# Performance work log

Hardware: AMD Instinct MI355X
Metric: run time of the kernel (lower is better)

The kernel has to match this reference:

```python
import jax, jax.numpy as jnp
import numpy as np

B, T, I, H = 32, 1024, 512, 512


def _uniform(key, shape, stdv):
    return jax.random.uniform(key, shape, jnp.float32, -stdv, stdv)


def setup_inputs() -> dict:
    key = jax.random.key(0)
    ks = jax.random.split(key, 13)
    stdv = 1.0 / np.sqrt(H)
    return {
        "z": jax.random.normal(ks[0], (B, T, I, 2), jnp.float32),
        "W_zi": _uniform(ks[1], (I, H, 2), stdv), "W_hi": _uniform(ks[2], (H, H, 2), stdv), "b_i": _uniform(ks[3], (H,), stdv),
        "W_zf": _uniform(ks[4], (I, H, 2), stdv), "W_hf": _uniform(ks[5], (H, H, 2), stdv), "b_f": _uniform(ks[6], (H,), stdv),
        "W_zc": _uniform(ks[7], (I, H, 2), stdv), "W_hc": _uniform(ks[8], (H, H, 2), stdv), "b_c": _uniform(ks[9], (H, 2), stdv),
        "W_zo": _uniform(ks[10], (I, H, 2), stdv), "W_ho": _uniform(ks[11], (H, H, 2), stdv), "b_o": _uniform(ks[12], (H,), stdv),
    }


def complex_tanh(zr, zi):
    mag = jnp.maximum(jnp.sqrt(zr * zr + zi * zi + 1e-14), 1e-8)
    t = jnp.tanh(mag)
    return t * (zr / mag), t * (zi / mag)


def reference(z, W_zi, W_hi, b_i, W_zf, W_hf, b_f, W_zc, W_hc, b_c, W_zo, W_ho, b_o):
    zr, zi = z[..., 0], z[..., 1]  # (B,T,I)

    def in_proj_real(Wz):  # real part of complex matmul z @ Wz
        return jnp.einsum('bti,ih->bth', zr, Wz[..., 0]) - jnp.einsum('bti,ih->bth', zi, Wz[..., 1])

    xi = in_proj_real(W_zi)
    xf = in_proj_real(W_zf)
    xo = in_proj_real(W_zo)
    xcr = in_proj_real(W_zc)
    xci = jnp.einsum('bti,ih->bth', zi, W_zc[..., 0]) + jnp.einsum('bti,ih->bth', zr, W_zc[..., 1])

    # time-major for scan: (T,B,H)
    xs = tuple(jnp.swapaxes(a, 0, 1) for a in (xi, xf, xo, xcr, xci))

    def step(carry, x):
        h_r, h_i, c_r, c_i = carry
        xi_t, xf_t, xo_t, xcr_t, xci_t = x
        i_t = jax.nn.sigmoid(xi_t + h_r @ W_hi[..., 0] - h_i @ W_hi[..., 1] + b_i)
        f_t = jax.nn.sigmoid(xf_t + h_r @ W_hf[..., 0] - h_i @ W_hf[..., 1] + b_f)
        o_t = jax.nn.sigmoid(xo_t + h_r @ W_ho[..., 0] - h_i @ W_ho[..., 1] + b_o)
        cr = xcr_t + h_r @ W_hc[..., 0] - h_i @ W_hc[..., 1] + b_c[..., 0]
        ci = xci_t + h_i @ W_hc[..., 0] + h_r @ W_hc[..., 1] + b_c[..., 1]
        ctr, cti = complex_tanh(cr, ci)
        c_r = f_t * c_r + i_t * ctr
        c_i = f_t * c_i + i_t * cti
        hr, hi = complex_tanh(c_r, c_i)
        h_r = o_t * hr
        h_i = o_t * hi
        return (h_r, h_i, c_r, c_i), jnp.stack((h_r, h_i), axis=-1)

    zero = jnp.zeros((z.shape[0], W_hi.shape[0]), z.dtype)
    (h_r, h_i, c_r, c_i), hs = jax.lax.scan(step, (zero, zero, zero, zero), xs)
    hidden_seq = jnp.swapaxes(hs, 0, 1)  # (B,T,H,2)
    h_t = jnp.stack((h_r, h_i), axis=-1)
    c_t = jnp.stack((c_r, c_i), axis=-1)
    return hidden_seq, (h_t, c_t)
```

## Files before the change

### kernel.cpp

```cpp
#include <hip/hip_runtime.h>


#define B_ 32
#define T_ 1024
#define Hd 512
#define Kd 1024
#define Nd 2560
#define Md 32768
#define HS_ELEMS 33554432ull

typedef __attribute__((ext_vector_type(8))) short bf16x8;
typedef __attribute__((ext_vector_type(4))) float f32x4;

__device__ __forceinline__ unsigned short f_bf(float f) {
  unsigned int x; __builtin_memcpy(&x, &f, 4);
  unsigned int r = (x + 0x7FFFu + ((x >> 16) & 1u)) >> 16;
  return (unsigned short)r;
}
__device__ __forceinline__ float bf_f(unsigned short u) {
  unsigned int i = ((unsigned int)u) << 16; float f; __builtin_memcpy(&f, &i, 4); return f;
}
__device__ __forceinline__ float fsig(float x) { return 1.0f / (1.0f + __expf(-x)); }
__device__ __forceinline__ void ctanh_(float zr, float zi, float& tr, float& ti) {
  float m2 = zr * zr + zi * zi + 1e-14f;
  float mag = __fsqrt_rn(m2);
  float e = __expf(2.0f * mag);
  float th = 1.0f - 2.0f / (e + 1.0f);
  float s = th / mag;
  tr = zr * s; ti = zi * s;
}

__device__ __forceinline__ void gl16(const unsigned short* g, unsigned short* l) {
  __builtin_amdgcn_global_load_lds(
      (const __attribute__((address_space(1))) void*)g,
      (__attribute__((address_space(3))) void*)l, 16, 0, 0);
}

__device__ __forceinline__ unsigned int ald(const unsigned int* p) {
  return __hip_atomic_load(p, __ATOMIC_RELAXED, __HIP_MEMORY_SCOPE_AGENT);
}
__device__ __forceinline__ void ast(unsigned int* p, unsigned int v) {
  __hip_atomic_store(p, v, __ATOMIC_RELAXED, __HIP_MEMORY_SCOPE_AGENT);
}

__global__ void build_weights(const float* Wzi, const float* Whi, const float* bi,
                              const float* Wzf, const float* Whf, const float* bfv,
                              const float* Wzc, const float* Whc, const float* bc,
                              const float* Wzo, const float* Who, const float* bo,
                              unsigned short* WzT, unsigned short* WhT, float* bcomb) {
  int n = blockIdx.x;
  int slab = n / 80, wi = n % 80, g = wi / 16, hh = slab * 16 + (wi & 15);
  const float *Wz, *Wh;
  if (g == 0)      { Wz = Wzi; Wh = Whi; }
  else if (g == 1) { Wz = Wzf; Wh = Whf; }
  else if (g == 2) { Wz = Wzo; Wh = Who; }
  else             { Wz = Wzc; Wh = Whc; }
  int q0, q1; float s0, s1;
  if (g < 4) { q0 = 0; s0 = 1.f; q1 = 1; s1 = -1.f; }
  else       { q0 = 1; s0 = 1.f; q1 = 0; s1 =  1.f; }
  for (int k = threadIdx.x; k < Kd; k += 256) {
    int j = k >> 1, p = k & 1;
    int q = p ? q1 : q0; float sg = p ? s1 : s0;
    WzT[(size_t)n * Kd + k] = f_bf(sg * Wz[(j * Hd + hh) * 2 + q]);
    WhT[(size_t)n * Kd + k] = f_bf(sg * Wh[(j * Hd + hh) * 2 + q]);
  }
  if (threadIdx.x == 0) {
    float bv;
    if (g == 0) bv = bi[hh]; else if (g == 1) bv = bfv[hh];
    else if (g == 2) bv = bo[hh];
    else if (g == 3) bv = bc[2 * hh]; else bv = bc[2 * hh + 1];
    bcomb[n] = bv;
  }
}

__global__ void cvt_z(const float4* __restrict__ z, ushort4* __restrict__ Z2) {
  for (size_t i = (size_t)blockIdx.x * 256 + threadIdx.x; i < 8388608ull; i += 8192ull * 256) {
    float4 v = z[i];
    ushort4 o;
    o.x = f_bf(v.x); o.y = f_bf(v.y); o.z = f_bf(v.z); o.w = f_bf(v.w);
    Z2[i] = o;
  }
}

__global__ __launch_bounds__(256) void gemm_x(const unsigned short* __restrict__ Z2,
                                              const unsigned short* __restrict__ WT,
                                              unsigned short* __restrict__ X) {
  __shared__ unsigned short As[128 * 64];
  __shared__ unsigned short Bs[128 * 64];
  int tid = threadIdx.x, lane = tid & 63, wv = tid >> 6;
  int bid = blockIdx.x;
  int mb = bid / (Nd / 128), nb = bid % (Nd / 128);
  size_t m0 = (size_t)mb * 128, n0 = (size_t)nb * 128;
  int wr = wv >> 1, wc = wv & 1;
  int l15 = lane & 15, kg = lane >> 4;
  int lrow = tid >> 3;
  int lcol = (tid & 7) * 8;
  f32x4 acc[4][4] = {};
  for (int k0 = 0; k0 < Kd; k0 += 64) {
    __syncthreads();
#pragma unroll
    for (int c = 0; c < 4; ++c) {
      gl16(Z2 + (m0 + c * 32 + lrow) * Kd + k0 + lcol,
           As + (size_t)c * 2048 + wv * 512);
      gl16(WT + (n0 + c * 32 + lrow) * Kd + k0 + lcol,
           Bs + (size_t)c * 2048 + wv * 512);
    }
    __syncthreads();
#pragma unroll
    for (int ks = 0; ks < 2; ++ks) {
      int kk = ks * 32 + kg * 8;
      bf16x8 a[4], b[4];
#pragma unroll
      for (int i = 0; i < 4; ++i)
        a[i] = *reinterpret_cast<const bf16x8*>(&As[(wr * 64 + i * 16 + l15) * 64 + kk]);
#pragma unroll
      for (int j = 0; j < 4; ++j)
        b[j] = *reinterpret_cast<const bf16x8*>(&Bs[(wc * 64 + j * 16 + l15) * 64 + kk]);
#pragma unroll
      for (int i = 0; i < 4; ++i)
#pragma unroll
        for (int j = 0; j < 4; ++j)
          acc[i][j] = __builtin_amdgcn_mfma_f32_16x16x32_bf16(a[i], b[j], acc[i][j], 0, 0, 0);
    }
  }
#pragma unroll
  for (int i = 0; i < 4; ++i)
#pragma unroll
    for (int j = 0; j < 4; ++j) {
      size_t gm = m0 + wr * 64 + i * 16 + kg * 4;
      size_t gn = n0 + wc * 64 + j * 16 + l15;
#pragma unroll
      for (int r = 0; r < 4; ++r)
        X[(gm + r) * Nd + gn] = f_bf(acc[i][j][r]);
    }
}

#define CHUNK 8
#define STEPB (Nd * 2)
__global__ __launch_bounds__(512) void lstm_all(
    const unsigned short* __restrict__ WhT, const unsigned short* __restrict__ X,
    const float* __restrict__ bcomb, unsigned short* __restrict__ hb,
    int* __restrict__ flags, float* __restrict__ out) {
  __shared__ unsigned short Xs[2][CHUNK * STEPB / 2];
  __shared__ float xch[8][5][256];
  const int s = blockIdx.x;
  const int tid = threadIdx.x;
  const int wv = tid >> 6, lane = tid & 63;
  const int kh = wv >> 1, mh = wv & 1;
  const int l15 = lane & 15, kg = lane >> 4;
  const int cb = tid >> 4;
  const int ch = tid & 15;
  const int hh = s * 16 + ch;

  auto stage = [&](int tbase, int buf) {
#pragma unroll
    for (int j = 0; j < 5; ++j) {
      unsigned int P = (unsigned int)(wv * 5 + j) * 1024u + (unsigned int)lane * 16u;
      unsigned int st = P / STEPB, r = P % STEPB;
      unsigned int b = r / 160u, rem = r % 160u;
      gl16(X + ((size_t)b * T_ + (tbase + st)) * Nd + s * 80 + rem / 2,
           &Xs[buf][(size_t)(wv * 5 + j) * 512]);
    }
  };
  stage(0, 0);

  bf16x8 w[5][8];
#pragma unroll
  for (int g = 0; g < 5; ++g)
#pragma unroll
    for (int ks = 0; ks < 8; ++ks)
      w[g][ks] = *reinterpret_cast<const bf16x8*>(
          &WhT[(size_t)(s * 80 + g * 16 + l15) * Kd + kh * 256 + ks * 32 + kg * 8]);

  float bias[5];
#pragma unroll
  for (int g = 0; g < 5; ++g) bias[g] = bcomb[s * 80 + g * 16 + ch];
  float cr = 0.f, ci = 0.f;

  const int fidx = kh * 8 + (lane & 7);
  const int mb = cb >> 4;
  const int xidx = ((cb & 15) >> 2) * 64 + ch * 4 + (cb & 3);

  float2 hist[8];

  for (int tb = 0; tb < T_; tb += 8) {
#pragma unroll
    for (int j = 0; j < 8; ++j) {
      const int t = tb + j;
      bf16x8 a[8];
      if (t > 0) {
        const unsigned int need = (unsigned int)(t + 1);
        while (true) {
          unsigned int v = ald((const unsigned int*)&flags[fidx]);
          if (__all(v >= need)) break;
        }
        asm volatile("" ::: "memory");

        const unsigned short* hin = hb + (size_t)(t % 3) * 32768;
        unsigned long long hpa = (unsigned long long)(
            hin + (size_t)(mh * 16 + l15) * Kd + kh * 256 + kg * 8);
#define HL(i, off) asm volatile("global_load_dwordx4 %0, %1, off offset:" #off " sc0 sc1" \
                                 : "=&v"(a[i]) : "v"(hpa) : "memory")
        HL(0, 0); HL(1, 64); HL(2, 128); HL(3, 192);
        HL(4, 256); HL(5, 320); HL(6, 384); HL(7, 448);
#undef HL
        asm volatile("s_waitcnt vmcnt(0)" ::: "memory");
        __builtin_amdgcn_sched_barrier(0);
      } else {
#pragma unroll
        for (int ks = 0; ks < 8; ++ks)
#pragma unroll
          for (int e = 0; e < 8; ++e) a[ks][e] = 0;
      }

      f32x4 acc[5] = {};
#pragma unroll
      for (int ks = 0; ks < 8; ++ks)
#pragma unroll
        for (int g = 0; g < 5; ++g)
          acc[g] = __builtin_amdgcn_mfma_f32_16x16x32_bf16(a[ks], w[g][ks], acc[g], 0, 0, 0);

#pragma unroll
      for (int g = 0; g < 5; ++g)
        *reinterpret_cast<f32x4*>(&xch[wv][g][lane * 4]) = acc[g];
      __syncthreads();

      const unsigned short* xsl = &Xs[(t >> 3) & 1][(t & 7) * Nd + cb * 80 + ch];
      float pre[5];
#pragma unroll
      for (int g = 0; g < 5; ++g) {
        float p = bias[g] + bf_f(xsl[g * 16]);
#pragma unroll
        for (int q = 0; q < 4; ++q) p += xch[q * 2 + mb][g][xidx];
        pre[g] = p;
      }
      float ig = fsig(pre[0]), fg = fsig(pre[1]), og = fsig(pre[2]);
      float ctr, cti; ctanh_(pre[3], pre[4], ctr, cti);
      cr = fg * cr + ig * ctr;
      ci = fg * ci + ig * cti;
      float hr0, hi0; ctanh_(cr, ci, hr0, hi0);
      float hr = og * hr0, hi = og * hi0;
      hist[j] = make_float2(hr, hi);

      unsigned int hv = (unsigned int)f_bf(hr) | ((unsigned int)f_bf(hi) << 16);
      ast((unsigned int*)hb + (size_t)((t + 1) % 3) * 16384 + (size_t)cb * 512 + hh, hv);
      if (t < T_ - 1) {
        asm volatile("s_waitcnt vmcnt(0)" ::: "memory");
        __syncthreads();
        if (tid == 0) ast((unsigned int*)&flags[s], (unsigned int)(t + 2));
      }

      if (j == 7) {
#pragma unroll
        for (int q = 0; q < 8; ++q) {
          size_t oidx = ((size_t)cb * T_ + (t - 7 + q)) * (Hd * 2) + hh * 2;
          *reinterpret_cast<float2*>(&out[oidx]) = hist[q];
        }
        if (t + 1 < T_) stage(t + 1, ((t + 1) >> 3) & 1);
      }
      if (t == T_ - 1) {
        size_t fb = HS_ELEMS + ((size_t)cb * Hd + hh) * 2;
        *reinterpret_cast<float2*>(&out[fb]) = make_float2(hr, hi);
        *reinterpret_cast<float2*>(&out[fb + 32768ull]) = make_float2(cr, ci);
      }
      __syncthreads();
    }
  }
}

extern "C" void kernel_launch(void* const* d_in, const int* in_sizes, int n_in,
                              void* d_out, int out_size, void* d_ws, size_t ws_size,
                              hipStream_t stream) {
  const float* z   = (const float*)d_in[0];
  const float* Wzi = (const float*)d_in[1];
  const float* Whi = (const float*)d_in[2];
  const float* bi  = (const float*)d_in[3];
  const float* Wzf = (const float*)d_in[4];
  const float* Whf = (const float*)d_in[5];
  const float* bfv = (const float*)d_in[6];
  const float* Wzc = (const float*)d_in[7];
  const float* Whc = (const float*)d_in[8];
  const float* bc  = (const float*)d_in[9];
  const float* Wzo = (const float*)d_in[10];
  const float* Who = (const float*)d_in[11];
  const float* bo  = (const float*)d_in[12];
  float* out = (float*)d_out;

  size_t off = 0;
  char* ws = (char*)d_ws;
  auto take = [&](size_t nbytes) {
    void* p = ws + off; off += (nbytes + 255) & ~(size_t)255; return p;
  };
  unsigned short* WzT  = (unsigned short*)take((size_t)Nd * Kd * 2);
  unsigned short* WhT  = (unsigned short*)take((size_t)Nd * Kd * 2);
  float*          bcmb = (float*)take(Nd * 4);
  unsigned short* Z2   = (unsigned short*)take((size_t)Md * Kd * 2);
  unsigned short* X    = (unsigned short*)take((size_t)Md * Nd * 2);
  unsigned short* hb   = (unsigned short*)take(3 * 32768 * 2);
  int*            flags = (int*)take(64 * 4);

  hipMemsetAsync(flags, 0, 64 * 4, stream);
  build_weights<<<Nd, 256, 0, stream>>>(Wzi, Whi, bi, Wzf, Whf, bfv,
                                        Wzc, Whc, bc, Wzo, Who, bo,
                                        WzT, WhT, bcmb);
  cvt_z<<<8192, 256, 0, stream>>>((const float4*)z, (ushort4*)Z2);
  gemm_x<<<(Md / 128) * (Nd / 128), 256, 0, stream>>>(Z2, WzT, X);
  lstm_all<<<32, 512, 0, stream>>>(WhT, X, bcmb, hb, flags, out);
}
```

Before: 5.339 ms.

## Overlap input-projection GEMM with recurrent LSTM via producer blocks in one launch

Merges the input-projection GEMM into the persistent LSTM kernel. 32 blocks run the recurrence while 224 extra blocks compute X tiles in time-chunk order and signal completion per 128-step chunk through atomic counters. The GEMM cost can then hide behind the serial recurrence instead of running before it. X staging is moved to the start of each 8-step group with a wait on chunk readiness, and one per-step __syncthreads is dropped. The risks are that the GEMM blocks contend with the latency-bound recurrent blocks for bandwidth, and that the GEMM blocks now use 512 threads with only half of them active.

Result: slower. 5.703 ms (+6.8%).

```diff
diff --git a/kernel.cpp b/kernel.cpp
--- a/kernel.cpp
+++ b/kernel.cpp
@@ -82,69 +82,88 @@
   }
 }
 
-__global__ __launch_bounds__(256) void gemm_x(const unsigned short* __restrict__ Z2,
-                                              const unsigned short* __restrict__ WT,
-                                              unsigned short* __restrict__ X) {
-  __shared__ unsigned short As[128 * 64];
-  __shared__ unsigned short Bs[128 * 64];
-  int tid = threadIdx.x, lane = tid & 63, wv = tid >> 6;
-  int bid = blockIdx.x;
-  int mb = bid / (Nd / 128), nb = bid % (Nd / 128);
-  size_t m0 = (size_t)mb * 128, n0 = (size_t)nb * 128;
-  int wr = wv >> 1, wc = wv & 1;
-  int l15 = lane & 15, kg = lane >> 4;
-  int lrow = tid >> 3;
-  int lcol = (tid & 7) * 8;
-  f32x4 acc[4][4] = {};
-  for (int k0 = 0; k0 < Kd; k0 += 64) {
-    __syncthreads();
-#pragma unroll
-    for (int c = 0; c < 4; ++c) {
-      gl16(Z2 + (m0 + c * 32 + lrow) * Kd + k0 + lcol,
-           As + (size_t)c * 2048 + wv * 512);
-      gl16(WT + (n0 + c * 32 + lrow) * Kd + k0 + lcol,
-           Bs + (size_t)c * 2048 + wv * 512);
-    }
-    __syncthreads();
-#pragma unroll
-    for (int ks = 0; ks < 2; ++ks) {
-      int kk = ks * 32 + kg * 8;
-      bf16x8 a[4], b[4];
-#pragma unroll
-      for (int i = 0; i < 4; ++i)
-        a[i] = *reinterpret_cast<const bf16x8*>(&As[(wr * 64 + i * 16 + l15) * 64 + kk]);
-#pragma unroll
-      for (int j = 0; j < 4; ++j)
-        b[j] = *reinterpret_cast<const bf16x8*>(&Bs[(wc * 64 + j * 16 + l15) * 64 + kk]);
-#pragma unroll
-      for (int i = 0; i < 4; ++i)
-#pragma unroll
-        for (int j = 0; j < 4; ++j)
-          acc[i][j] = __builtin_amdgcn_mfma_f32_16x16x32_bf16(a[i], b[j], acc[i][j], 0, 0, 0);
-    }
-  }
-#pragma unroll
-  for (int i = 0; i < 4; ++i)
-#pragma unroll
-    for (int j = 0; j < 4; ++j) {
-      size_t gm = m0 + wr * 64 + i * 16 + kg * 4;
-      size_t gn = n0 + wc * 64 + j * 16 + l15;
-#pragma unroll
-      for (int r = 0; r < 4; ++r)
-        X[(gm + r) * Nd + gn] = f_bf(acc[i][j][r]);
-    }
-}
-
 #define CHUNK 8
 #define STEPB (Nd * 2)
 __global__ __launch_bounds__(512) void lstm_all(
-    const unsigned short* __restrict__ WhT, const unsigned short* __restrict__ X,
+    const unsigned short* __restrict__ WhT, unsigned short* __restrict__ X,
+    const unsigned short* __restrict__ Z2, const unsigned short* __restrict__ WzT,
     const float* __restrict__ bcomb, unsigned short* __restrict__ hb,
-    int* __restrict__ flags, float* __restrict__ out) {
+    int* __restrict__ ctl, float* __restrict__ out) {
   __shared__ unsigned short Xs[2][CHUNK * STEPB / 2];
   __shared__ float xch[8][5][256];
+  __shared__ unsigned short As[128 * 64];
+  __shared__ unsigned short Bs[128 * 64];
   const int s = blockIdx.x;
   const int tid = threadIdx.x;
+  unsigned int* bc = (unsigned int*)(ctl + 32);
+
+  if (s >= 32) {
+    const int lane = tid & 63, wvg = tid >> 6;
+    const int wr = wvg >> 1, wc = wvg & 1;
+    const int l15 = lane & 15, kg = lane >> 4;
+    const int lrow = tid >> 3;
+    const int lcol = (tid & 7) * 8;
+    for (int tau = s - 32; tau < 5120; tau += 224) {
+      int tb8 = tau / 640, rr = tau % 640;
+      int mb = (rr / 20) * 8 + tb8, nb = rr % 20;
+      size_t m0 = (size_t)mb * 128, n0 = (size_t)nb * 128;
+      f32x4 acc[4][4] = {};
+      for (int k0 = 0; k0 < Kd; k0 += 64) {
+        __syncthreads();
+        if (tid < 256) {
+#pragma unroll
+          for (int c = 0; c < 4; ++c) {
+            gl16(Z2 + (m0 + c * 32 + lrow) * Kd + k0 + lcol,
+                 As + (size_t)c * 2048 + wvg * 512);
+            gl16(WzT + (n0 + c * 32 + lrow) * Kd + k0 + lcol,
+                 Bs + (size_t)c * 2048 + wvg * 512);
+          }
+        }
+        __syncthreads();
+        if (tid < 256) {
+#pragma unroll
+          for (int ks = 0; ks < 2; ++ks) {
+            int kk = ks * 32 + kg * 8;
+            bf16x8 a[4], b[4];
+#pragma unroll
+            for (int i = 0; i < 4; ++i)
+              a[i] = *reinterpret_cast<const bf16x8*>(&As[(wr * 64 + i * 16 + l15) * 64 + kk]);
+#pragma unroll
+            for (int j = 0; j < 4; ++j)
+              b[j] = *reinterpret_cast<const bf16x8*>(&Bs[(wc * 64 + j * 16 + l15) * 64 + kk]);
+#pragma unroll
+            for (int i = 0; i < 4; ++i)
+#pragma unroll
+              for (int j = 0; j < 4; ++j)
+                acc[i][j] = __builtin_amdgcn_mfma_f32_16x16x32_bf16(a[i], b[j], acc[i][j], 0, 0, 0);
+          }
+        }
+      }
+      if (tid < 256) {
+#pragma unroll
+        for (int i = 0; i < 4; ++i)
+#pragma unroll
+          for (int j = 0; j < 4; ++j) {
+            size_t gm = m0 + wr * 64 + i * 16 + kg * 4;
+            size_t gn = n0 + wc * 64 + j * 16 + l15;
+#pragma unroll
+            for (int r = 0; r < 4; ++r) {
+              unsigned int v = f_bf(acc[i][j][r]);
+              const unsigned short* p = X + (gm + r) * Nd + gn;
+              asm volatile("global_store_short %0, %1, off sc0 sc1"
+                           :: "v"(p), "v"(v) : "memory");
+            }
+          }
+        asm volatile("s_waitcnt vmcnt(0)" ::: "memory");
+      }
+      __syncthreads();
+      if (tid == 0)
+        __hip_atomic_fetch_add((int*)&bc[tb8], 1, __ATOMIC_RELAXED,
+                               __HIP_MEMORY_SCOPE_AGENT);
+    }
+    return;
+  }
+
   const int wv = tid >> 6, lane = tid & 63;
   const int kh = wv >> 1, mh = wv & 1;
   const int l15 = lane & 15, kg = lane >> 4;
@@ -162,6 +181,12 @@
            &Xs[buf][(size_t)(wv * 5 + j) * 512]);
     }
   };
+  auto waitblk = [&](int t8) {
+    while (ald(&bc[t8 >> 7]) < 640u) {}
+    asm volatile("" ::: "memory");
+  };
+
+  waitblk(0);
   stage(0, 0);
 
   bf16x8 w[5][8];
@@ -191,7 +216,7 @@
       if (t > 0) {
         const unsigned int need = (unsigned int)(t + 1);
         while (true) {
-          unsigned int v = ald((const unsigned int*)&flags[fidx]);
+          unsigned int v = ald((const unsigned int*)&ctl[fidx]);
           if (__all(v >= need)) break;
         }
         asm volatile("" ::: "memory");
@@ -213,6 +238,11 @@
           for (int e = 0; e < 8; ++e) a[ks][e] = 0;
       }
 
+      if (j == 0 && t + 8 < T_) {
+        if (((t + 8) & 127) == 0) waitblk(t + 8);
+        stage(t + 8, ((t >> 3) + 1) & 1);
+      }
+
       f32x4 acc[5] = {};
 #pragma unroll
       for (int ks = 0; ks < 8; ++ks)
@@ -247,7 +277,7 @@
       if (t < T_ - 1) {
         asm volatile("s_waitcnt vmcnt(0)" ::: "memory");
         __syncthreads();
-        if (tid == 0) ast((unsigned int*)&flags[s], (unsigned int)(t + 2));
+        if (tid == 0) ast((unsigned int*)&ctl[s], (unsigned int)(t + 2));
       }
 
       if (j == 7) {
@@ -256,14 +286,12 @@
           size_t oidx = ((size_t)cb * T_ + (t - 7 + q)) * (Hd * 2) + hh * 2;
           *reinterpret_cast<float2*>(&out[oidx]) = hist[q];
         }
-        if (t + 1 < T_) stage(t + 1, ((t + 1) >> 3) & 1);
       }
       if (t == T_ - 1) {
         size_t fb = HS_ELEMS + ((size_t)cb * Hd + hh) * 2;
         *reinterpret_cast<float2*>(&out[fb]) = make_float2(hr, hi);
         *reinterpret_cast<float2*>(&out[fb + 32768ull]) = make_float2(cr, ci);
       }
-      __syncthreads();
     }
   }
 }
@@ -297,13 +325,12 @@
   unsigned short* Z2   = (unsigned short*)take((size_t)Md * Kd * 2);
   unsigned short* X    = (unsigned short*)take((size_t)Md * Nd * 2);
   unsigned short* hb   = (unsigned short*)take(3 * 32768 * 2);
-  int*            flags = (int*)take(64 * 4);
-
-  hipMemsetAsync(flags, 0, 64 * 4, stream);
+  int*            ctl  = (int*)take(4096);
+
+  hipMemsetAsync(ctl, 0, 4096, stream);
   build_weights<<<Nd, 256, 0, stream>>>(Wzi, Whi, bi, Wzf, Whf, bfv,
                                         Wzc, Whc, bc, Wzo, Who, bo,
                                         WzT, WhT, bcmb);
   cvt_z<<<8192, 256, 0, stream>>>((const float4*)z, (ushort4*)Z2);
-  gemm_x<<<(Md / 128) * (Nd / 128), 256, 0, stream>>>(Z2, WzT, X);
-  lstm_all<<<32, 512, 0, stream>>>(WhT, X, bcmb, hb, flags, out);
-}
+  lstm_all<<<256, 512, 0, stream>>>(WhT, X, Z2, WzT, bcmb, hb, ctl, out);
+}
```

## Tag hidden-state words with timestep to skip flag polling in recurrence

Applied to the files above, without the earlier changes.

Each hidden-state bf16 value is stored in its own 32-bit word with the timestep in the upper 16 bits. A consumer first loads the data and checks the tags, and only falls back to polling the per-block flags and reloading when some tag is stale. This takes the flag spin-wait off the critical path of each recurrent step. It also moves the X staging for the next chunk to the start of the chunk and drops the trailing per-step barrier. In exchange the hidden-state exchange buffer doubles in size and needs a memset, and each step does twice as many global loads plus unpacking.

Result: slower. 9.622 ms (+80.2%).

```diff
diff --git a/kernel.cpp b/kernel.cpp
--- a/kernel.cpp
+++ b/kernel.cpp
@@ -8,6 +8,7 @@
 #define Nd 2560
 #define Md 32768
 #define HS_ELEMS 33554432ull
+#define HSLOT 32768
 
 typedef __attribute__((ext_vector_type(8))) short bf16x8;
 typedef __attribute__((ext_vector_type(4))) float f32x4;
@@ -139,7 +140,7 @@
 #define STEPB (Nd * 2)
 __global__ __launch_bounds__(512) void lstm_all(
     const unsigned short* __restrict__ WhT, const unsigned short* __restrict__ X,
-    const float* __restrict__ bcomb, unsigned short* __restrict__ hb,
+    const float* __restrict__ bcomb, unsigned int* __restrict__ hb,
     int* __restrict__ flags, float* __restrict__ out) {
   __shared__ unsigned short Xs[2][CHUNK * STEPB / 2];
   __shared__ float xch[8][5][256];
@@ -177,6 +178,10 @@
   for (int g = 0; g < 5; ++g) bias[g] = bcomb[s * 80 + g * 16 + ch];
   float cr = 0.f, ci = 0.f;
 
+  const unsigned int cdw = (unsigned int)(mh * 16 + l15) * 1024u
+                           + (unsigned int)(kh * 256 + kg * 8);
+  const unsigned int pdw = (unsigned int)cb * 1024u + 2u * (unsigned int)hh;
+
   const int fidx = kh * 8 + (lane & 7);
   const int mb = cb >> 4;
   const int xidx = ((cb & 15) >> 2) * 64 + ch * 4 + (cb & 3);
@@ -189,23 +194,47 @@
       const int t = tb + j;
       bf16x8 a[8];
       if (t > 0) {
-        const unsigned int need = (unsigned int)(t + 1);
-        while (true) {
-          unsigned int v = ald((const unsigned int*)&flags[fidx]);
-          if (__all(v >= need)) break;
+        const unsigned int tagw = (unsigned int)t << 16;
+        unsigned long long hpb = (unsigned long long)(hb + (size_t)(t % 3) * HSLOT + cdw);
+        uint4 u0[8], u1[8];
+#define HL(dst, OFFS) asm volatile("global_load_dwordx4 %0, %1, off offset:" OFFS " sc0 sc1" \
+                                   : "=&v"(dst) : "v"(hpb) : "memory")
+#define LOADALL() do { \
+        HL(u0[0], "0");   HL(u1[0], "16");  HL(u0[1], "128"); HL(u1[1], "144"); \
+        HL(u0[2], "256"); HL(u1[2], "272"); HL(u0[3], "384"); HL(u1[3], "400"); \
+        HL(u0[4], "512"); HL(u1[4], "528"); HL(u0[5], "640"); HL(u1[5], "656"); \
+        HL(u0[6], "768"); HL(u1[6], "784"); HL(u0[7], "896"); HL(u1[7], "912"); \
+        asm volatile("s_waitcnt vmcnt(0)" ::: "memory"); \
+        __builtin_amdgcn_sched_barrier(0); } while (0)
+        LOADALL();
+        unsigned int bad = 0;
+#pragma unroll
+        for (int q = 0; q < 8; ++q) {
+          bad |= (u0[q].x ^ tagw) & 0xFFFF0000u; bad |= (u0[q].y ^ tagw) & 0xFFFF0000u;
+          bad |= (u0[q].z ^ tagw) & 0xFFFF0000u; bad |= (u0[q].w ^ tagw) & 0xFFFF0000u;
+          bad |= (u1[q].x ^ tagw) & 0xFFFF0000u; bad |= (u1[q].y ^ tagw) & 0xFFFF0000u;
+          bad |= (u1[q].z ^ tagw) & 0xFFFF0000u; bad |= (u1[q].w ^ tagw) & 0xFFFF0000u;
         }
-        asm volatile("" ::: "memory");
-
-        const unsigned short* hin = hb + (size_t)(t % 3) * 32768;
-        unsigned long long hpa = (unsigned long long)(
-            hin + (size_t)(mh * 16 + l15) * Kd + kh * 256 + kg * 8);
-#define HL(i, off) asm volatile("global_load_dwordx4 %0, %1, off offset:" #off " sc0 sc1" \
-                                 : "=&v"(a[i]) : "v"(hpa) : "memory")
-        HL(0, 0); HL(1, 64); HL(2, 128); HL(3, 192);
-        HL(4, 256); HL(5, 320); HL(6, 384); HL(7, 448);
+        if (!__all(bad == 0)) {
+          const unsigned int need = (unsigned int)(t + 1);
+          while (true) {
+            unsigned int v = ald((const unsigned int*)&flags[fidx]);
+            if (__all(v >= need)) break;
+          }
+          asm volatile("" ::: "memory");
+          LOADALL();
+        }
+#undef LOADALL
 #undef HL
-        asm volatile("s_waitcnt vmcnt(0)" ::: "memory");
-        __builtin_amdgcn_sched_barrier(0);
+#pragma unroll
+        for (int q = 0; q < 8; ++q) {
+          union { bf16x8 v; unsigned int d[4]; } ua;
+          ua.d[0] = (u0[q].x & 0xFFFFu) | (u0[q].y << 16);
+          ua.d[1] = (u0[q].z & 0xFFFFu) | (u0[q].w << 16);
+          ua.d[2] = (u1[q].x & 0xFFFFu) | (u1[q].y << 16);
+          ua.d[3] = (u1[q].z & 0xFFFFu) | (u1[q].w << 16);
+          a[q] = ua.v;
+        }
       } else {
 #pragma unroll
         for (int ks = 0; ks < 8; ++ks)
@@ -242,8 +271,12 @@
       float hr = og * hr0, hi = og * hi0;
       hist[j] = make_float2(hr, hi);
 
-      unsigned int hv = (unsigned int)f_bf(hr) | ((unsigned int)f_bf(hi) << 16);
-      ast((unsigned int*)hb + (size_t)((t + 1) % 3) * 16384 + (size_t)cb * 512 + hh, hv);
+      {
+        unsigned int tn = (unsigned int)(t + 1) << 16;
+        unsigned int* hp = hb + (size_t)((t + 1) % 3) * HSLOT + pdw;
+        ast(hp,     (unsigned int)f_bf(hr) | tn);
+        ast(hp + 1, (unsigned int)f_bf(hi) | tn);
+      }
       if (t < T_ - 1) {
         asm volatile("s_waitcnt vmcnt(0)" ::: "memory");
         __syncthreads();
@@ -256,14 +289,13 @@
           size_t oidx = ((size_t)cb * T_ + (t - 7 + q)) * (Hd * 2) + hh * 2;
           *reinterpret_cast<float2*>(&out[oidx]) = hist[q];
         }
-        if (t + 1 < T_) stage(t + 1, ((t + 1) >> 3) & 1);
-      }
+      }
+      if (j == 0 && t + 8 < T_) stage(t + 8, ((t >> 3) + 1) & 1);
       if (t == T_ - 1) {
         size_t fb = HS_ELEMS + ((size_t)cb * Hd + hh) * 2;
         *reinterpret_cast<float2*>(&out[fb]) = make_float2(hr, hi);
         *reinterpret_cast<float2*>(&out[fb + 32768ull]) = make_float2(cr, ci);
       }
-      __syncthreads();
     }
   }
 }
@@ -296,10 +328,11 @@
   float*          bcmb = (float*)take(Nd * 4);
   unsigned short* Z2   = (unsigned short*)take((size_t)Md * Kd * 2);
   unsigned short* X    = (unsigned short*)take((size_t)Md * Nd * 2);
-  unsigned short* hb   = (unsigned short*)take(3 * 32768 * 2);
-  int*            flags = (int*)take(64 * 4);
-
-  hipMemsetAsync(flags, 0, 64 * 4, stream);
+  unsigned int*   hb   = (unsigned int*)take(3 * HSLOT * 4);
+  int*            flags = (int*)take(256);
+
+  hipMemsetAsync(hb, 0, 3 * HSLOT * 4, stream);
+  hipMemsetAsync(flags, 0, 256, stream);
   build_weights<<<Nd, 256, 0, stream>>>(Wzi, Whi, bi, Wzf, Whf, bfv,
                                         Wzc, Whc, bc, Wzo, Who, bo,
                                         WzT, WhT, bcmb);
```
